# Kernel optimization log

Measured on AMD Instinct MI355X. Metric: run time of the kernel, lower is better.

## Reference

```python
import jax, jax.numpy as jnp
import numpy as np

C = 256
EPS = 1e-5

def setup_inputs() -> dict:
    key = jax.random.key(0)
    ks = jax.random.split(key, 10)
    N, H, W = 4, 64, 64
    Ch = C // 2
    sc = 1.0 / np.sqrt(C)
    sch = 1.0 / np.sqrt(Ch)
    return {
        "x": jax.random.normal(ks[0], (N, C, H, W), dtype=jnp.float32),
        "cfc": jax.random.normal(ks[1], (C, 2), dtype=jnp.float32) * 0.1,
        "theta_w": jax.random.normal(ks[2], (Ch, C), dtype=jnp.float32) * sc,
        "theta_b": jax.random.normal(ks[3], (Ch,), dtype=jnp.float32) * 0.01,
        "phi_w": jax.random.normal(ks[4], (Ch, C), dtype=jnp.float32) * sc,
        "phi_b": jax.random.normal(ks[5], (Ch,), dtype=jnp.float32) * 0.01,
        "g_w": jax.random.normal(ks[6], (Ch, C), dtype=jnp.float32) * sc,
        "g_b": jax.random.normal(ks[7], (Ch,), dtype=jnp.float32) * 0.01,
        "out_w": jax.random.normal(ks[8], (C, Ch), dtype=jnp.float32) * sch,
        "out_b": jax.random.normal(ks[9], (C,), dtype=jnp.float32) * 0.01,
    }

def reference(x, cfc, theta_w, theta_b, phi_w, phi_b, g_w, g_b, out_w, out_b):
    N, Cc, H, W = x.shape
    L = H * W
    xf = x.reshape(N, Cc, L)
    # SRM style pooling: per-channel mean and (unbiased) std over spatial dims
    mean = jnp.mean(xf, axis=2)                              # [N,C]
    var = jnp.var(xf, axis=2, ddof=1) + EPS                  # torch .var() is unbiased
    std = jnp.sqrt(var)
    # style integration: z = mean*cfc[:,0] + std*cfc[:,1], gate = sigmoid(z)
    z = mean * cfc[None, :, 0] + std * cfc[None, :, 1]       # [N,C]
    gate = jax.nn.sigmoid(z)[:, :, None]                     # [N,C,1]
    s = xf * gate                                            # srm_out flattened [N,C,L]
    # 1x1 convs == per-pixel linear maps
    theta = jnp.einsum('oc,ncl->nol', theta_w, s) + theta_b[None, :, None]  # [N,C/2,L]
    phi = jnp.einsum('oc,ncl->nol', phi_w, s) + phi_b[None, :, None]
    g = jnp.einsum('oc,ncl->nol', g_w, s) + g_b[None, :, None]
    # attention[n,i,j] = sum_c theta[n,c,i]*phi[n,c,j]; softmax over j (no 1/sqrt(d))
    attn = jax.nn.softmax(jnp.einsum('nci,ncj->nij', theta, phi), axis=-1)  # [N,L,L]
    # nl_out[n,c,i] = sum_j g[n,c,j]*attn[n,i,j]
    nl = jnp.einsum('ncj,nij->nci', g, attn)                 # [N,C/2,L]
    nl = jnp.einsum('oc,ncl->nol', out_w, nl) + out_b[None, :, None]        # [N,C,L]
    out = s + nl
    return out.reshape(N, Cc, H, W)
```

## Files before the change

### kernel.cpp

```cpp
#include <hip/hip_runtime.h>
#include <hip/hip_bf16.h>

#define LSP 4096
#define NC  256
#define NH  128
#define KB  64
#define SPLIT 4
#define NTILE ((LSP / SPLIT) / KB)

typedef __attribute__((ext_vector_type(8))) short short8;
typedef __attribute__((ext_vector_type(4))) float f32x4;
typedef __attribute__((ext_vector_type(4))) unsigned int u32x4;
typedef __attribute__((ext_vector_type(2))) unsigned int u32x2;
typedef __attribute__((ext_vector_type(4))) unsigned short u16x4;
typedef __hip_bfloat16 bf16;

#define MFMA16(a,b,c) __builtin_amdgcn_mfma_f32_16x16x32_bf16((a),(b),(c),0,0,0)

typedef __attribute__((address_space(1))) const void gas_t;
typedef __attribute__((address_space(3))) void las_t;
#define GLDS16(g, l) __builtin_amdgcn_global_load_lds((gas_t*)(g), (las_t*)(l), 16, 0, 0)

static __device__ __forceinline__ unsigned short f2bf(float f) {
  bf16 h = __float2bfloat16(f);
  return __builtin_bit_cast(unsigned short, h);
}
static __device__ __forceinline__ unsigned int packbf2(float a, float b) {
  return (unsigned int)f2bf(a) | ((unsigned int)f2bf(b) << 16);
}
static __device__ __forceinline__ float bf2f(unsigned short u) {
  return __builtin_bit_cast(float, (unsigned int)u << 16);
}

__global__ __launch_bounds__(256) void k_wconv(const float* __restrict__ a0,
    const float* __restrict__ a1, const float* __restrict__ a2,
    const float* __restrict__ a3, const float* __restrict__ tb,
    const float* __restrict__ pb, bf16* __restrict__ dst, float* __restrict__ bcat) {
  int i = blockIdx.x * 256 + threadIdx.x;
  int seg = i >> 15, off = i & 32767;
  const float* s = (seg == 0) ? a0 : (seg == 1) ? a1 : (seg == 2) ? a2 : a3;
  dst[i] = __float2bfloat16(s[off]);
  if (blockIdx.x == 0)
    bcat[threadIdx.x] = threadIdx.x < 128 ? tb[threadIdx.x] : pb[threadIdx.x - 128];
}

__global__ __launch_bounds__(256) void k_stats(const float* __restrict__ x,
    const float* __restrict__ cfc, float* __restrict__ gate) {
  int nc = blockIdx.x;
  const float4* x4 = (const float4*)(x + (size_t)nc * LSP);
  float s = 0.f, q = 0.f;
  for (int i = threadIdx.x; i < LSP / 4; i += 256) {
    float4 v = x4[i];
    s += v.x + v.y + v.z + v.w;
    q += v.x * v.x + v.y * v.y + v.z * v.z + v.w * v.w;
  }
#pragma unroll
  for (int o = 32; o > 0; o >>= 1) { s += __shfl_xor(s, o); q += __shfl_xor(q, o); }
  __shared__ float rs[4], rq[4];
  int w = threadIdx.x >> 6;
  if ((threadIdx.x & 63) == 0) { rs[w] = s; rq[w] = q; }
  __syncthreads();
  if (threadIdx.x == 0) {
    float S = rs[0] + rs[1] + rs[2] + rs[3];
    float Q = rq[0] + rq[1] + rq[2] + rq[3];
    float mean = S / (float)LSP;
    float var = (Q - S * S / (float)LSP) / (float)(LSP - 1) + 1e-5f;
    float sd = sqrtf(var);
    int c = nc & (NC - 1);
    float z = mean * cfc[2 * c] + sd * cfc[2 * c + 1];
    gate[nc] = 1.f / (1.f + __expf(-z));
  }
}

__global__ __launch_bounds__(256) void k_scale_t(const float* __restrict__ x,
    const float* __restrict__ gate, bf16* __restrict__ s_t) {
  int n = blockIdx.z;
  int c0 = blockIdx.y * 32;
  int l = blockIdx.x * 256 + threadIdx.x;
  unsigned int pk[16];
#pragma unroll
  for (int i = 0; i < 32; i += 2) {
    int c = c0 + i;
    float g0 = gate[n * NC + c];
    float g1 = gate[n * NC + c + 1];
    float v0 = x[((size_t)(n * NC + c)) * LSP + l] * g0;
    float v1 = x[((size_t)(n * NC + c + 1)) * LSP + l] * g1;
    pk[i >> 1] = packbf2(v0, v1);
  }
  u32x4* dst = (u32x4*)(s_t + ((size_t)n * LSP + l) * NC + c0);
#pragma unroll
  for (int k = 0; k < 4; ++k) dst[k] = ((const u32x4*)pk)[k];
}

__global__ __launch_bounds__(256) void k_gemm_nt(const bf16* __restrict__ A,
    const bf16* __restrict__ B, const float* __restrict__ bias, int bias_row,
    bf16* __restrict__ D, int Md, int Nd, int Kd, long sA, long sB, long sD) {
  int z = blockIdx.z;
  A += (size_t)z * sA; B += (size_t)z * sB; D += (size_t)z * sD;
  int tn = Nd >> 6;
  int m0 = (blockIdx.x / tn) * 64, n0 = (blockIdx.x % tn) * 64;
  int tid = threadIdx.x, w = tid >> 6, lane = tid & 63;
  int lo = lane & 15, g = lane >> 4;
  f32x4 zero = {0.f, 0.f, 0.f, 0.f};
  f32x4 acc[4];
#pragma unroll
  for (int i = 0; i < 4; ++i) acc[i] = zero;
  for (int kc = 0; kc < Kd; kc += 32) {
    short8 bfr = *(const short8*)(B + (size_t)(n0 + w * 16 + lo) * Kd + kc + g * 8);
#pragma unroll
    for (int i = 0; i < 4; ++i) {
      short8 afr = *(const short8*)(A + (size_t)(m0 + 16 * i + lo) * Kd + kc + g * 8);
      acc[i] = MFMA16(afr, bfr, acc[i]);
    }
  }
  int col = n0 + w * 16 + lo;
#pragma unroll
  for (int i = 0; i < 4; ++i)
#pragma unroll
    for (int r = 0; r < 4; ++r) {
      int row = m0 + 16 * i + g * 4 + r;
      float bv = bias_row ? bias[row] : bias[col];
      D[(size_t)row * Nd + col] = __float2bfloat16(acc[i][r] + bv);
    }
}

__global__ __launch_bounds__(256, 2) void k_attn(const bf16* __restrict__ thph,
    const bf16* __restrict__ gT, bf16* __restrict__ Opart, float* __restrict__ ml) {
  __shared__ bf16 Kl[2][KB * NH];
  __shared__ bf16 Vl[2][NH * KB];
  __shared__ bf16 Pl[4][32 * KB];

  const int n = blockIdx.z, sp = blockIdx.y;
  const int tid = threadIdx.x, w = tid >> 6, lane = tid & 63;
  const int lo = lane & 15, g = lane >> 4;
  const int swz = (lo & 7) << 4;

  const bf16* thn = thph + (size_t)n * LSP * 256;
  const bf16* gv  = gT + (size_t)n * NH * LSP;
  const int q0 = blockIdx.x * 128 + w * 32;
  const int j0base = sp * (LSP / SPLIT);

  short8 qf[2][4];
#pragma unroll
  for (int qs = 0; qs < 2; ++qs)
#pragma unroll
    for (int kc = 0; kc < 4; ++kc)
      qf[qs][kc] = *(const short8*)(thn + (size_t)(q0 + qs * 16 + lo) * 256 + kc * 32 + g * 8);

  size_t koff[4], voff[4];
  int ldso[4];
#pragma unroll
  for (int i = 0; i < 4; ++i) {
    int ci = i * 256 + tid;
    int kj = ci >> 4, kcc = ci & 15;
    koff[i] = (size_t)kj * 256 + 128 + ((kcc ^ (kj & 7)) * 8);
    int vd = ci >> 3, vc2 = ci & 7;
    voff[i] = (size_t)vd * LSP + ((vc2 ^ (vd & 7)) * 8);
    ldso[i] = ci * 16;
  }

#define STAGE(JT, BUF) do { \
    const bf16* ksrc = thn + (size_t)(j0base + (JT) * KB) * 256; \
    const bf16* vsrc = gv + (j0base + (JT) * KB); \
    char* kdst = (char*)&Kl[BUF][0]; \
    char* vdst = (char*)&Vl[BUF][0]; \
    _Pragma("unroll") \
    for (int i = 0; i < 4; ++i) { \
      GLDS16(ksrc + koff[i], kdst + ldso[i]); \
      GLDS16(vsrc + voff[i], vdst + ldso[i]); \
    } } while (0)

  f32x4 zero = {0.f, 0.f, 0.f, 0.f};
  f32x4 acc[2][8];
#pragma unroll
  for (int qs = 0; qs < 2; ++qs)
#pragma unroll
    for (int dc = 0; dc < 8; ++dc) acc[qs][dc] = zero;
  float mv[2] = {-1e30f, -1e30f};
  float ls[2] = {0.f, 0.f};

  STAGE(0, 0);
  __syncthreads();

  char* pwb = (char*)&Pl[w][0];

  for (int t = 0; t < NTILE; ++t) {
    int cur = t & 1;
    if (t + 1 < NTILE) STAGE(t + 1, cur ^ 1);
    const char* Kb = (const char*)&Kl[cur][0];
    const char* Vb = (const char*)&Vl[cur][0];

    f32x4 st[2][4];
#pragma unroll
    for (int qs = 0; qs < 2; ++qs)
#pragma unroll
      for (int jt = 0; jt < 4; ++jt) st[qs][jt] = zero;
#pragma unroll
    for (int kc = 0; kc < 4; ++kc) {
      int kb = (kc * 64 + g * 16) ^ swz;
#pragma unroll
      for (int jt = 0; jt < 4; ++jt) {
        short8 ka = *(const short8*)(Kb + (jt * 16 + lo) * 256 + kb);
        st[0][jt] = MFMA16(ka, qf[0][kc], st[0][jt]);
        st[1][jt] = MFMA16(ka, qf[1][kc], st[1][jt]);
      }
    }

    float tm[2];
#pragma unroll
    for (int qs = 0; qs < 2; ++qs) {
      float t0 = fmaxf(fmaxf(st[qs][0][0], st[qs][0][1]), fmaxf(st[qs][0][2], st[qs][0][3]));
      float t1 = fmaxf(fmaxf(st[qs][1][0], st[qs][1][1]), fmaxf(st[qs][1][2], st[qs][1][3]));
      float t2 = fmaxf(fmaxf(st[qs][2][0], st[qs][2][1]), fmaxf(st[qs][2][2], st[qs][2][3]));
      float t3 = fmaxf(fmaxf(st[qs][3][0], st[qs][3][1]), fmaxf(st[qs][3][2], st[qs][3][3]));
      float tq = fmaxf(fmaxf(t0, t1), fmaxf(t2, t3));
      tq = fmaxf(tq, __shfl_xor(tq, 16));
      tq = fmaxf(tq, __shfl_xor(tq, 32));
      tm[qs] = tq;
    }

    int need = (tm[0] > mv[0] + 8.f) || (tm[1] > mv[1] + 8.f);
    if (__any(need)) {
      float nm0 = fmaxf(mv[0], tm[0]), nm1 = fmaxf(mv[1], tm[1]);
      float a0 = __expf(mv[0] - nm0), a1 = __expf(mv[1] - nm1);
      mv[0] = nm0; mv[1] = nm1; ls[0] *= a0; ls[1] *= a1;
#pragma unroll
      for (int r = 0; r < 4; ++r) {
        float b0 = __shfl(a0, g * 4 + r);
        float b1 = __shfl(a1, g * 4 + r);
#pragma unroll
        for (int dc = 0; dc < 8; ++dc) { acc[0][dc][r] *= b0; acc[1][dc][r] *= b1; }
      }
    }

#pragma unroll
    for (int qs = 0; qs < 2; ++qs) {
      float mm = mv[qs];
      float psum = 0.f;
      int rowb = (qs * 16 + lo) * 128;
#pragma unroll
      for (int jt = 0; jt < 4; ++jt) {
        float e0 = __expf(st[qs][jt][0] - mm);
        float e1 = __expf(st[qs][jt][1] - mm);
        float e2 = __expf(st[qs][jt][2] - mm);
        float e3 = __expf(st[qs][jt][3] - mm);
        psum += (e0 + e1) + (e2 + e3);
        u32x2 pk;
        pk.x = packbf2(e0, e1);
        pk.y = packbf2(e2, e3);
        *(u32x2*)(pwb + rowb + ((jt * 32 + g * 8) ^ swz)) = pk;
      }
      psum += __shfl_xor(psum, 16);
      psum += __shfl_xor(psum, 32);
      ls[qs] += psum;
    }

    asm volatile("" ::: "memory");
#pragma unroll
    for (int kc2 = 0; kc2 < 2; ++kc2) {
      int kbb = kc2 * 64 + g * 16;
      short8 pa0 = *(const short8*)(pwb + lo * 128 + (kbb ^ swz));
      short8 pa1 = *(const short8*)(pwb + (16 + lo) * 128 + (kbb ^ swz));
#pragma unroll
      for (int dc = 0; dc < 8; ++dc) {
        int d = dc * 16 + lo;
        short8 vb = *(const short8*)(Vb + d * 128 + (kbb ^ ((d & 7) << 4)));
        acc[0][dc] = MFMA16(pa0, vb, acc[0][dc]);
        acc[1][dc] = MFMA16(pa1, vb, acc[1][dc]);
      }
    }
    __syncthreads();
  }

  bf16* opb = Opart + ((size_t)(sp * 4 + n) * LSP + q0) * NH;
#pragma unroll
  for (int qs = 0; qs < 2; ++qs)
#pragma unroll
    for (int dc = 0; dc < 8; ++dc)
#pragma unroll
      for (int r = 0; r < 4; ++r)
        opb[(size_t)(qs * 16 + g * 4 + r) * NH + dc * 16 + lo] =
            __float2bfloat16(acc[qs][dc][r]);
  if (g == 0) {
    float2* mlp = (float2*)ml + (size_t)(sp * 4 + n) * LSP + q0;
    mlp[lo] = make_float2(mv[0], ls[0]);
    mlp[16 + lo] = make_float2(mv[1], ls[1]);
  }
#undef STAGE
}

__global__ __launch_bounds__(256) void k_comb(const bf16* __restrict__ Opart,
    const float* __restrict__ ml, bf16* __restrict__ O_t) {
  int t = blockIdx.x * 256 + threadIdx.x;
  int nl = t >> 5, d0 = (t & 31) * 4;
  float2 m4[SPLIT];
  float mx = -1e30f;
#pragma unroll
  for (int s = 0; s < SPLIT; ++s) {
    m4[s] = ((const float2*)ml)[(size_t)s * (4 * LSP) + nl];
    mx = fmaxf(mx, m4[s].x);
  }
  float den = 0.f, ws[SPLIT];
#pragma unroll
  for (int s = 0; s < SPLIT; ++s) {
    ws[s] = __expf(m4[s].x - mx);
    den += m4[s].y * ws[s];
  }
  float inv = 1.f / den;
  float o0 = 0.f, o1 = 0.f, o2 = 0.f, o3 = 0.f;
#pragma unroll
  for (int s = 0; s < SPLIT; ++s) {
    u16x4 v = *(const u16x4*)(Opart + ((size_t)s * (4 * LSP) + nl) * NH + d0);
    float sc = ws[s] * inv;
    o0 += bf2f(v.x) * sc; o1 += bf2f(v.y) * sc;
    o2 += bf2f(v.z) * sc; o3 += bf2f(v.w) * sc;
  }
  u32x2 pk;
  pk.x = packbf2(o0, o1);
  pk.y = packbf2(o2, o3);
  *(u32x2*)(O_t + (size_t)nl * NH + d0) = pk;
}

__global__ __launch_bounds__(256) void k_final(const bf16* __restrict__ Wo,
    const bf16* __restrict__ O_t, const float* __restrict__ x,
    const float* __restrict__ gate, const float* __restrict__ ob,
    float* __restrict__ out) {
  int n = blockIdx.z;
  int m0 = (blockIdx.x >> 6) * 64, n0 = (blockIdx.x & 63) * 64;
  int tid = threadIdx.x, w = tid >> 6, lane = tid & 63;
  int lo = lane & 15, g = lane >> 4;
  const bf16* Bp = O_t + (size_t)n * LSP * NH;
  f32x4 zero = {0.f, 0.f, 0.f, 0.f};
  f32x4 acc[4];
#pragma unroll
  for (int i = 0; i < 4; ++i) acc[i] = zero;
  int col = n0 + w * 16 + lo;
#pragma unroll
  for (int kc = 0; kc < 4; ++kc) {
    short8 bfr = *(const short8*)(Bp + (size_t)col * NH + kc * 32 + g * 8);
#pragma unroll
    for (int i = 0; i < 4; ++i) {
      short8 afr = *(const short8*)(Wo + (size_t)(m0 + 16 * i + lo) * NH + kc * 32 + g * 8);
      acc[i] = MFMA16(afr, bfr, acc[i]);
    }
  }
#pragma unroll
  for (int i = 0; i < 4; ++i)
#pragma unroll
    for (int r = 0; r < 4; ++r) {
      int c = m0 + 16 * i + g * 4 + r;
      size_t xo = ((size_t)(n * NC + c)) * LSP + col;
      out[xo] = acc[i][r] + ob[c] + x[xo] * gate[n * NC + c];
    }
}

extern "C" void kernel_launch(void* const* d_in, const int* in_sizes, int n_in,
                              void* d_out, int out_size, void* d_ws, size_t ws_size,
                              hipStream_t stream) {
  const float* x       = (const float*)d_in[0];
  const float* cfc     = (const float*)d_in[1];
  const float* theta_w = (const float*)d_in[2];
  const float* theta_b = (const float*)d_in[3];
  const float* phi_w   = (const float*)d_in[4];
  const float* phi_b   = (const float*)d_in[5];
  const float* g_w     = (const float*)d_in[6];
  const float* g_b     = (const float*)d_in[7];
  const float* out_w   = (const float*)d_in[8];
  const float* out_b   = (const float*)d_in[9];
  float* out = (float*)d_out;

  char* p = (char*)d_ws;
  auto alloc = [&](size_t bytes) { char* r = p; p += (bytes + 255) & ~(size_t)255; return r; };
  float* gate  = (float*)alloc(4 * NC * sizeof(float));
  bf16* s_t    = (bf16*)alloc((size_t)4 * LSP * NC * 2);
  bf16* thph   = (bf16*)alloc((size_t)4 * LSP * 256 * 2);
  bf16* gTb    = (bf16*)alloc((size_t)4 * NH * LSP * 2);
  bf16* O_t    = (bf16*)alloc((size_t)4 * LSP * NH * 2);
  bf16* wbf    = (bf16*)alloc((size_t)4 * 32768 * 2);
  float* bcat  = (float*)alloc(256 * sizeof(float));
  bf16* Opart  = (bf16*)alloc((size_t)SPLIT * 4 * LSP * NH * 2);
  float* ml    = (float*)alloc((size_t)SPLIT * 4 * LSP * 2 * 4);

  k_wconv<<<512, 256, 0, stream>>>(theta_w, phi_w, g_w, out_w, theta_b, phi_b, wbf, bcat);
  k_stats<<<4 * NC, 256, 0, stream>>>(x, cfc, gate);
  k_scale_t<<<dim3(16, 8, 4), 256, 0, stream>>>(x, gate, s_t);

  k_gemm_nt<<<dim3(256, 1, 4), 256, 0, stream>>>(s_t, wbf, bcat, 0, thph,
      LSP, 256, NC, (long)LSP * NC, 0, (long)LSP * 256);
  k_gemm_nt<<<dim3(128, 1, 4), 256, 0, stream>>>(wbf + 65536, s_t, g_b, 1, gTb,
      NH, LSP, NC, 0, (long)LSP * NC, (long)NH * LSP);

  k_attn<<<dim3(LSP / 128, SPLIT, 4), 256, 0, stream>>>(thph, gTb, Opart, ml);
  k_comb<<<(4 * LSP * 32) / 256, 256, 0, stream>>>(Opart, ml, O_t);
  k_final<<<dim3(256, 1, 4), 256, 0, stream>>>(wbf + 98304, O_t, x, gate, out_b, out);
}
```

Baseline: 198.8 us.

## Fuse prep and GEMM launches, widen attention tile, triple-buffer, fold combine into final

```diff
diff --git a/kernel.cpp b/kernel.cpp
--- a/kernel.cpp
+++ b/kernel.cpp
@@ -5,6 +5,7 @@
 #define NC  256
 #define NH  128
 #define KB  64
+#define QW  64
 #define SPLIT 4
 #define NTILE ((LSP / SPLIT) / KB)
 
@@ -12,7 +13,6 @@
 typedef __attribute__((ext_vector_type(4))) float f32x4;
 typedef __attribute__((ext_vector_type(4))) unsigned int u32x4;
 typedef __attribute__((ext_vector_type(2))) unsigned int u32x2;
-typedef __attribute__((ext_vector_type(4))) unsigned short u16x4;
 typedef __hip_bfloat16 bf16;
 
 #define MFMA16(a,b,c) __builtin_amdgcn_mfma_f32_16x16x32_bf16((a),(b),(c),0,0,0)
@@ -32,21 +32,23 @@
   return __builtin_bit_cast(float, (unsigned int)u << 16);
 }
 
-__global__ __launch_bounds__(256) void k_wconv(const float* __restrict__ a0,
+__global__ __launch_bounds__(256) void k_pre(const float* __restrict__ a0,
     const float* __restrict__ a1, const float* __restrict__ a2,
     const float* __restrict__ a3, const float* __restrict__ tb,
-    const float* __restrict__ pb, bf16* __restrict__ dst, float* __restrict__ bcat) {
-  int i = blockIdx.x * 256 + threadIdx.x;
-  int seg = i >> 15, off = i & 32767;
-  const float* s = (seg == 0) ? a0 : (seg == 1) ? a1 : (seg == 2) ? a2 : a3;
-  dst[i] = __float2bfloat16(s[off]);
-  if (blockIdx.x == 0)
-    bcat[threadIdx.x] = threadIdx.x < 128 ? tb[threadIdx.x] : pb[threadIdx.x - 128];
-}
-
-__global__ __launch_bounds__(256) void k_stats(const float* __restrict__ x,
-    const float* __restrict__ cfc, float* __restrict__ gate) {
-  int nc = blockIdx.x;
+    const float* __restrict__ pb, bf16* __restrict__ dst, float* __restrict__ bcat,
+    const float* __restrict__ x, const float* __restrict__ cfc,
+    float* __restrict__ gate) {
+  int b = blockIdx.x;
+  if (b < 512) {
+    int i = b * 256 + threadIdx.x;
+    int seg = i >> 15, off = i & 32767;
+    const float* s = (seg == 0) ? a0 : (seg == 1) ? a1 : (seg == 2) ? a2 : a3;
+    dst[i] = __float2bfloat16(s[off]);
+    if (b == 0)
+      bcat[threadIdx.x] = threadIdx.x < 128 ? tb[threadIdx.x] : pb[threadIdx.x - 128];
+    return;
+  }
+  int nc = b - 512;
   const float4* x4 = (const float4*)(x + (size_t)nc * LSP);
   float s = 0.f, q = 0.f;
   for (int i = threadIdx.x; i < LSP / 4; i += 256) {
@@ -92,13 +94,11 @@
   for (int k = 0; k < 4; ++k) dst[k] = ((const u32x4*)pk)[k];
 }
 
-__global__ __launch_bounds__(256) void k_gemm_nt(const bf16* __restrict__ A,
+static __device__ __forceinline__ void gemm_nt_body(const bf16* __restrict__ A,
     const bf16* __restrict__ B, const float* __restrict__ bias, int bias_row,
-    bf16* __restrict__ D, int Md, int Nd, int Kd, long sA, long sB, long sD) {
-  int z = blockIdx.z;
-  A += (size_t)z * sA; B += (size_t)z * sB; D += (size_t)z * sD;
+    bf16* __restrict__ D, int Nd, int Kd, int bx) {
   int tn = Nd >> 6;
-  int m0 = (blockIdx.x / tn) * 64, n0 = (blockIdx.x % tn) * 64;
+  int m0 = (bx / tn) * 64, n0 = (bx % tn) * 64;
   int tid = threadIdx.x, w = tid >> 6, lane = tid & 63;
   int lo = lane & 15, g = lane >> 4;
   f32x4 zero = {0.f, 0.f, 0.f, 0.f};
@@ -124,11 +124,24 @@
     }
 }
 
-__global__ __launch_bounds__(256, 2) void k_attn(const bf16* __restrict__ thph,
+__global__ __launch_bounds__(256) void k_gemms(const bf16* __restrict__ s_t,
+    const bf16* __restrict__ wbf, const float* __restrict__ bcat,
+    const float* __restrict__ g_b, bf16* __restrict__ thph, bf16* __restrict__ gTb) {
+  int z = blockIdx.z, bx = blockIdx.x;
+  if (bx < 256) {
+    gemm_nt_body(s_t + (size_t)z * LSP * NC, wbf, bcat, 0,
+                 thph + (size_t)z * LSP * 256, 256, NC, bx);
+  } else {
+    gemm_nt_body(wbf + 65536, s_t + (size_t)z * LSP * NC, g_b, 1,
+                 gTb + (size_t)z * NH * LSP, LSP, NC, bx - 256);
+  }
+}
+
+__global__ __launch_bounds__(256, 1) void k_attn(const bf16* __restrict__ thph,
     const bf16* __restrict__ gT, bf16* __restrict__ Opart, float* __restrict__ ml) {
-  __shared__ bf16 Kl[2][KB * NH];
-  __shared__ bf16 Vl[2][NH * KB];
-  __shared__ bf16 Pl[4][32 * KB];
+  __shared__ bf16 Kl[3][KB * NH];
+  __shared__ bf16 Vl[3][NH * KB];
+  __shared__ bf16 Pl[4][QW * KB];
 
   const int n = blockIdx.z, sp = blockIdx.y;
   const int tid = threadIdx.x, w = tid >> 6, lane = tid & 63;
@@ -137,12 +150,12 @@
 
   const bf16* thn = thph + (size_t)n * LSP * 256;
   const bf16* gv  = gT + (size_t)n * NH * LSP;
-  const int q0 = blockIdx.x * 128 + w * 32;
+  const int q0 = blockIdx.x * 256 + w * QW;
   const int j0base = sp * (LSP / SPLIT);
 
-  short8 qf[2][4];
-#pragma unroll
-  for (int qs = 0; qs < 2; ++qs)
+  short8 qf[4][4];
+#pragma unroll
+  for (int qs = 0; qs < 4; ++qs)
 #pragma unroll
     for (int kc = 0; kc < 4; ++kc)
       qf[qs][kc] = *(const short8*)(thn + (size_t)(q0 + qs * 16 + lo) * 256 + kc * 32 + g * 8);
@@ -171,79 +184,76 @@
     } } while (0)
 
   f32x4 zero = {0.f, 0.f, 0.f, 0.f};
-  f32x4 acc[2][8];
-#pragma unroll
-  for (int qs = 0; qs < 2; ++qs)
+  f32x4 acc[4][8];
+#pragma unroll
+  for (int qs = 0; qs < 4; ++qs)
 #pragma unroll
     for (int dc = 0; dc < 8; ++dc) acc[qs][dc] = zero;
-  float mv[2] = {-1e30f, -1e30f};
-  float ls[2] = {0.f, 0.f};
+  float mv[4] = {-1e30f, -1e30f, -1e30f, -1e30f};
+  float ls[4] = {0.f, 0.f, 0.f, 0.f};
 
   STAGE(0, 0);
-  __syncthreads();
+  STAGE(1, 1);
 
   char* pwb = (char*)&Pl[w][0];
 
   for (int t = 0; t < NTILE; ++t) {
-    int cur = t & 1;
-    if (t + 1 < NTILE) STAGE(t + 1, cur ^ 1);
+    int cur = t % 3;
+    if (t < NTILE - 1) asm volatile("s_waitcnt vmcnt(8)" ::: "memory");
+    else               asm volatile("s_waitcnt vmcnt(0)" ::: "memory");
+    __builtin_amdgcn_sched_barrier(0);
+    __builtin_amdgcn_s_barrier();
+    if (t + 2 < NTILE) STAGE(t + 2, (t + 2) % 3);
+
     const char* Kb = (const char*)&Kl[cur][0];
     const char* Vb = (const char*)&Vl[cur][0];
 
-    f32x4 st[2][4];
-#pragma unroll
-    for (int qs = 0; qs < 2; ++qs)
-#pragma unroll
-      for (int jt = 0; jt < 4; ++jt) st[qs][jt] = zero;
-#pragma unroll
-    for (int kc = 0; kc < 4; ++kc) {
-      int kb = (kc * 64 + g * 16) ^ swz;
-#pragma unroll
-      for (int jt = 0; jt < 4; ++jt) {
-        short8 ka = *(const short8*)(Kb + (jt * 16 + lo) * 256 + kb);
-        st[0][jt] = MFMA16(ka, qf[0][kc], st[0][jt]);
-        st[1][jt] = MFMA16(ka, qf[1][kc], st[1][jt]);
-      }
-    }
-
-    float tm[2];
-#pragma unroll
-    for (int qs = 0; qs < 2; ++qs) {
-      float t0 = fmaxf(fmaxf(st[qs][0][0], st[qs][0][1]), fmaxf(st[qs][0][2], st[qs][0][3]));
-      float t1 = fmaxf(fmaxf(st[qs][1][0], st[qs][1][1]), fmaxf(st[qs][1][2], st[qs][1][3]));
-      float t2 = fmaxf(fmaxf(st[qs][2][0], st[qs][2][1]), fmaxf(st[qs][2][2], st[qs][2][3]));
-      float t3 = fmaxf(fmaxf(st[qs][3][0], st[qs][3][1]), fmaxf(st[qs][3][2], st[qs][3][3]));
+    short8 kfr[4][4];
+#pragma unroll
+    for (int jt = 0; jt < 4; ++jt)
+#pragma unroll
+      for (int kc = 0; kc < 4; ++kc)
+        kfr[jt][kc] = *(const short8*)(Kb + (jt * 16 + lo) * 256 + ((kc * 64 + g * 16) ^ swz));
+
+#pragma unroll
+    for (int qs = 0; qs < 4; ++qs) {
+      f32x4 st[4];
+#pragma unroll
+      for (int jt = 0; jt < 4; ++jt) st[jt] = zero;
+#pragma unroll
+      for (int kc = 0; kc < 4; ++kc)
+#pragma unroll
+        for (int jt = 0; jt < 4; ++jt)
+          st[jt] = MFMA16(kfr[jt][kc], qf[qs][kc], st[jt]);
+
+      float t0 = fmaxf(fmaxf(st[0][0], st[0][1]), fmaxf(st[0][2], st[0][3]));
+      float t1 = fmaxf(fmaxf(st[1][0], st[1][1]), fmaxf(st[1][2], st[1][3]));
+      float t2 = fmaxf(fmaxf(st[2][0], st[2][1]), fmaxf(st[2][2], st[2][3]));
+      float t3 = fmaxf(fmaxf(st[3][0], st[3][1]), fmaxf(st[3][2], st[3][3]));
       float tq = fmaxf(fmaxf(t0, t1), fmaxf(t2, t3));
       tq = fmaxf(tq, __shfl_xor(tq, 16));
       tq = fmaxf(tq, __shfl_xor(tq, 32));
-      tm[qs] = tq;
-    }
-
-    int need = (tm[0] > mv[0] + 8.f) || (tm[1] > mv[1] + 8.f);
-    if (__any(need)) {
-      float nm0 = fmaxf(mv[0], tm[0]), nm1 = fmaxf(mv[1], tm[1]);
-      float a0 = __expf(mv[0] - nm0), a1 = __expf(mv[1] - nm1);
-      mv[0] = nm0; mv[1] = nm1; ls[0] *= a0; ls[1] *= a1;
-#pragma unroll
-      for (int r = 0; r < 4; ++r) {
-        float b0 = __shfl(a0, g * 4 + r);
-        float b1 = __shfl(a1, g * 4 + r);
-#pragma unroll
-        for (int dc = 0; dc < 8; ++dc) { acc[0][dc][r] *= b0; acc[1][dc][r] *= b1; }
+
+      if (__any(tq > mv[qs] + 8.f)) {
+        float nm = fmaxf(mv[qs], tq);
+        float a = __expf(mv[qs] - nm);
+        mv[qs] = nm; ls[qs] *= a;
+#pragma unroll
+        for (int r = 0; r < 4; ++r) {
+          float b = __shfl(a, g * 4 + r);
+#pragma unroll
+          for (int dc = 0; dc < 8; ++dc) acc[qs][dc][r] *= b;
+        }
       }
-    }
-
-#pragma unroll
-    for (int qs = 0; qs < 2; ++qs) {
-      float mm = mv[qs];
-      float psum = 0.f;
+
+      float mm = mv[qs], psum = 0.f;
       int rowb = (qs * 16 + lo) * 128;
 #pragma unroll
       for (int jt = 0; jt < 4; ++jt) {
-        float e0 = __expf(st[qs][jt][0] - mm);
-        float e1 = __expf(st[qs][jt][1] - mm);
-        float e2 = __expf(st[qs][jt][2] - mm);
-        float e3 = __expf(st[qs][jt][3] - mm);
+        float e0 = __expf(st[jt][0] - mm);
+        float e1 = __expf(st[jt][1] - mm);
+        float e2 = __expf(st[jt][2] - mm);
+        float e3 = __expf(st[jt][3] - mm);
         psum += (e0 + e1) + (e2 + e3);
         u32x2 pk;
         pk.x = packbf2(e0, e1);
@@ -259,22 +269,24 @@
 #pragma unroll
     for (int kc2 = 0; kc2 < 2; ++kc2) {
       int kbb = kc2 * 64 + g * 16;
-      short8 pa0 = *(const short8*)(pwb + lo * 128 + (kbb ^ swz));
-      short8 pa1 = *(const short8*)(pwb + (16 + lo) * 128 + (kbb ^ swz));
+      short8 pa[4];
+#pragma unroll
+      for (int qs = 0; qs < 4; ++qs)
+        pa[qs] = *(const short8*)(pwb + (qs * 16 + lo) * 128 + (kbb ^ swz));
 #pragma unroll
       for (int dc = 0; dc < 8; ++dc) {
         int d = dc * 16 + lo;
         short8 vb = *(const short8*)(Vb + d * 128 + (kbb ^ ((d & 7) << 4)));
-        acc[0][dc] = MFMA16(pa0, vb, acc[0][dc]);
-        acc[1][dc] = MFMA16(pa1, vb, acc[1][dc]);
+#pragma unroll
+        for (int qs = 0; qs < 4; ++qs)
+          acc[qs][dc] = MFMA16(pa[qs], vb, acc[qs][dc]);
       }
     }
-    __syncthreads();
   }
 
   bf16* opb = Opart + ((size_t)(sp * 4 + n) * LSP + q0) * NH;
 #pragma unroll
-  for (int qs = 0; qs < 2; ++qs)
+  for (int qs = 0; qs < 4; ++qs)
 #pragma unroll
     for (int dc = 0; dc < 8; ++dc)
 #pragma unroll
@@ -283,61 +295,58 @@
             __float2bfloat16(acc[qs][dc][r]);
   if (g == 0) {
     float2* mlp = (float2*)ml + (size_t)(sp * 4 + n) * LSP + q0;
-    mlp[lo] = make_float2(mv[0], ls[0]);
-    mlp[16 + lo] = make_float2(mv[1], ls[1]);
+#pragma unroll
+    for (int qs = 0; qs < 4; ++qs)
+      mlp[qs * 16 + lo] = make_float2(mv[qs], ls[qs]);
   }
 #undef STAGE
 }
 
-__global__ __launch_bounds__(256) void k_comb(const bf16* __restrict__ Opart,
-    const float* __restrict__ ml, bf16* __restrict__ O_t) {
-  int t = blockIdx.x * 256 + threadIdx.x;
-  int nl = t >> 5, d0 = (t & 31) * 4;
-  float2 m4[SPLIT];
-  float mx = -1e30f;
-#pragma unroll
-  for (int s = 0; s < SPLIT; ++s) {
-    m4[s] = ((const float2*)ml)[(size_t)s * (4 * LSP) + nl];
-    mx = fmaxf(mx, m4[s].x);
-  }
-  float den = 0.f, ws[SPLIT];
-#pragma unroll
-  for (int s = 0; s < SPLIT; ++s) {
-    ws[s] = __expf(m4[s].x - mx);
-    den += m4[s].y * ws[s];
-  }
-  float inv = 1.f / den;
-  float o0 = 0.f, o1 = 0.f, o2 = 0.f, o3 = 0.f;
-#pragma unroll
-  for (int s = 0; s < SPLIT; ++s) {
-    u16x4 v = *(const u16x4*)(Opart + ((size_t)s * (4 * LSP) + nl) * NH + d0);
-    float sc = ws[s] * inv;
-    o0 += bf2f(v.x) * sc; o1 += bf2f(v.y) * sc;
-    o2 += bf2f(v.z) * sc; o3 += bf2f(v.w) * sc;
-  }
-  u32x2 pk;
-  pk.x = packbf2(o0, o1);
-  pk.y = packbf2(o2, o3);
-  *(u32x2*)(O_t + (size_t)nl * NH + d0) = pk;
-}
-
 __global__ __launch_bounds__(256) void k_final(const bf16* __restrict__ Wo,
-    const bf16* __restrict__ O_t, const float* __restrict__ x,
-    const float* __restrict__ gate, const float* __restrict__ ob,
-    float* __restrict__ out) {
+    const bf16* __restrict__ Opart, const float* __restrict__ ml,
+    const float* __restrict__ x, const float* __restrict__ gate,
+    const float* __restrict__ ob, float* __restrict__ out) {
   int n = blockIdx.z;
   int m0 = (blockIdx.x >> 6) * 64, n0 = (blockIdx.x & 63) * 64;
   int tid = threadIdx.x, w = tid >> 6, lane = tid & 63;
   int lo = lane & 15, g = lane >> 4;
-  const bf16* Bp = O_t + (size_t)n * LSP * NH;
+  int col = n0 + w * 16 + lo;
+
+  float sc[SPLIT];
+  {
+    float2 m4[SPLIT];
+    float mx = -1e30f;
+#pragma unroll
+    for (int s = 0; s < SPLIT; ++s) {
+      m4[s] = ((const float2*)ml)[(size_t)(s * 4 + n) * LSP + col];
+      mx = fmaxf(mx, m4[s].x);
+    }
+    float den = 0.f;
+#pragma unroll
+    for (int s = 0; s < SPLIT; ++s) { sc[s] = __expf(m4[s].x - mx); den += m4[s].y * sc[s]; }
+    float inv = 1.f / den;
+#pragma unroll
+    for (int s = 0; s < SPLIT; ++s) sc[s] *= inv;
+  }
+
   f32x4 zero = {0.f, 0.f, 0.f, 0.f};
   f32x4 acc[4];
 #pragma unroll
   for (int i = 0; i < 4; ++i) acc[i] = zero;
-  int col = n0 + w * 16 + lo;
 #pragma unroll
   for (int kc = 0; kc < 4; ++kc) {
-    short8 bfr = *(const short8*)(Bp + (size_t)col * NH + kc * 32 + g * 8);
+    float bv[8] = {0.f, 0.f, 0.f, 0.f, 0.f, 0.f, 0.f, 0.f};
+#pragma unroll
+    for (int s = 0; s < SPLIT; ++s) {
+      short8 v = *(const short8*)(Opart + ((size_t)(s * 4 + n) * LSP + col) * NH + kc * 32 + g * 8);
+#pragma unroll
+      for (int e = 0; e < 8; ++e)
+        bv[e] += sc[s] * bf2f((unsigned short)v[e]);
+    }
+    u32x4 pk4;
+    pk4.x = packbf2(bv[0], bv[1]); pk4.y = packbf2(bv[2], bv[3]);
+    pk4.z = packbf2(bv[4], bv[5]); pk4.w = packbf2(bv[6], bv[7]);
+    short8 bfr = __builtin_bit_cast(short8, pk4);
 #pragma unroll
     for (int i = 0; i < 4; ++i) {
       short8 afr = *(const short8*)(Wo + (size_t)(m0 + 16 * i + lo) * NH + kc * 32 + g * 8);
@@ -375,22 +384,15 @@
   bf16* s_t    = (bf16*)alloc((size_t)4 * LSP * NC * 2);
   bf16* thph   = (bf16*)alloc((size_t)4 * LSP * 256 * 2);
   bf16* gTb    = (bf16*)alloc((size_t)4 * NH * LSP * 2);
-  bf16* O_t    = (bf16*)alloc((size_t)4 * LSP * NH * 2);
   bf16* wbf    = (bf16*)alloc((size_t)4 * 32768 * 2);
   float* bcat  = (float*)alloc(256 * sizeof(float));
   bf16* Opart  = (bf16*)alloc((size_t)SPLIT * 4 * LSP * NH * 2);
   float* ml    = (float*)alloc((size_t)SPLIT * 4 * LSP * 2 * 4);
 
-  k_wconv<<<512, 256, 0, stream>>>(theta_w, phi_w, g_w, out_w, theta_b, phi_b, wbf, bcat);
-  k_stats<<<4 * NC, 256, 0, stream>>>(x, cfc, gate);
+  k_pre<<<1536, 256, 0, stream>>>(theta_w, phi_w, g_w, out_w, theta_b, phi_b,
+                                  wbf, bcat, x, cfc, gate);
   k_scale_t<<<dim3(16, 8, 4), 256, 0, stream>>>(x, gate, s_t);
-
-  k_gemm_nt<<<dim3(256, 1, 4), 256, 0, stream>>>(s_t, wbf, bcat, 0, thph,
-      LSP, 256, NC, (long)LSP * NC, 0, (long)LSP * 256);
-  k_gemm_nt<<<dim3(128, 1, 4), 256, 0, stream>>>(wbf + 65536, s_t, g_b, 1, gTb,
-      NH, LSP, NC, 0, (long)LSP * NC, (long)NH * LSP);
-
-  k_attn<<<dim3(LSP / 128, SPLIT, 4), 256, 0, stream>>>(thph, gTb, Opart, ml);
-  k_comb<<<(4 * LSP * 32) / 256, 256, 0, stream>>>(Opart, ml, O_t);
-  k_final<<<dim3(256, 1, 4), 256, 0, stream>>>(wbf + 98304, O_t, x, gate, out_b, out);
-}
+  k_gemms<<<dim3(384, 1, 4), 256, 0, stream>>>(s_t, wbf, bcat, g_b, thph, gTb);
+  k_attn<<<dim3(LSP / 256, SPLIT, 4), 256, 0, stream>>>(thph, gTb, Opart, ml);
+  k_final<<<dim3(256, 1, 4), 256, 0, stream>>>(wbf + 98304, Opart, ml, x, gate, out_b, out);
+}
```

Measured after the change: 213.0 us. +7.1%, slower.
